# Kernel tuning notes

Hardware: AMD Instinct MI355X
Metric: run time of the kernel (lower is better)

The kernel has to match this reference:

```python
import jax, jax.numpy as jnp
import numpy as np

N_NODES = 20000
N_EDGES = 640000
HIDDEN = 128
NUM_FILTERS = 128
NUM_RBF = 50
NUM_LAYERS = 6
MAX_Z = 100
CUTOFF_UPPER = 5.0
CUTOFF_LOWER = 0.0


def _cosine_cutoff(d):
    # torchmd CosineCutoff with cutoff_lower == 0
    c = 0.5 * (jnp.cos(d * jnp.pi / CUTOFF_UPPER) + 1.0)
    return c * (d < CUTOFF_UPPER).astype(d.dtype)


def setup_inputs() -> dict:
    key = jax.random.key(0)
    ks = jax.random.split(key, 16)
    s = 0.05
    z = jax.random.randint(ks[0], (N_NODES,), 0, MAX_Z)
    pos = jax.random.uniform(ks[1], (N_NODES, 3), dtype=jnp.float32) * 3.0
    src = jax.random.randint(ks[2], (N_EDGES,), 0, N_NODES)
    off = jax.random.randint(ks[3], (N_EDGES,), 1, N_NODES)
    dst = (src + off) % N_NODES  # no self loops -> d > 0 a.s.
    edge_index = jnp.stack([src, dst])
    batch = jnp.zeros((N_NODES,), dtype=jnp.int32)
    # expnorm RBF initial params (ExpNormalSmearing._initial_params)
    start = float(np.exp(-CUTOFF_UPPER + CUTOFF_LOWER))
    rbf_means = jnp.linspace(start, 1.0, NUM_RBF, dtype=jnp.float32)
    rbf_betas = jnp.full((NUM_RBF,), (2.0 / NUM_RBF * (1.0 - start)) ** -2, dtype=jnp.float32)

    def w(k, shape):
        return jax.random.normal(k, shape, dtype=jnp.float32) * s

    L = NUM_LAYERS
    return dict(
        z=z, pos=pos, edge_index=edge_index, batch=batch,
        emb_table=w(ks[4], (MAX_Z, HIDDEN)),
        nbr_emb_table=w(ks[5], (MAX_Z, HIDDEN)),
        nbr_proj_W=w(ks[6], (NUM_RBF, HIDDEN)),
        nbr_proj_b=jnp.zeros((HIDDEN,), jnp.float32),
        combine_W=w(ks[7], (2 * HIDDEN, HIDDEN)),
        combine_b=jnp.zeros((HIDDEN,), jnp.float32),
        rbf_means=rbf_means, rbf_betas=rbf_betas,
        mlp_W1=w(ks[8], (L, NUM_RBF, NUM_FILTERS)),
        mlp_b1=jnp.zeros((L, NUM_FILTERS), jnp.float32),
        mlp_W2=w(ks[9], (L, NUM_FILTERS, NUM_FILTERS)),
        mlp_b2=jnp.zeros((L, NUM_FILTERS), jnp.float32),
        lin1_W=w(ks[10], (L, HIDDEN, NUM_FILTERS)),
        lin2_W=w(ks[11], (L, NUM_FILTERS, HIDDEN)),
        lin2_b=jnp.zeros((L, HIDDEN), jnp.float32),
        lin_W=w(ks[12], (L, HIDDEN, HIDDEN)),
        lin_b=jnp.zeros((L, HIDDEN), jnp.float32),
    )


def reference(z, pos, edge_index, batch, emb_table, nbr_emb_table,
              nbr_proj_W, nbr_proj_b, combine_W, combine_b,
              rbf_means, rbf_betas,
              mlp_W1, mlp_b1, mlp_W2, mlp_b2,
              lin1_W, lin2_W, lin2_b, lin_W, lin_b):
    src, dst = edge_index[0], edge_index[1]
    # Distance (loop=False): edge_vec = pos[src] - pos[dst]
    vec = pos[src] - pos[dst]                      # [E, 3]
    d = jnp.sqrt(jnp.sum(vec * vec, axis=-1))      # [E]
    C = _cosine_cutoff(d)                          # [E]
    alpha = 5.0 / (CUTOFF_UPPER - CUTOFF_LOWER)
    # ExpNormalSmearing: C(d) * exp(-beta * (exp(alpha*(-d+low)) - mu)^2)
    edge_attr = C[:, None] * jnp.exp(
        -rbf_betas * (jnp.exp(alpha * (-d[:, None] + CUTOFF_LOWER)) - rbf_means) ** 2
    )                                              # [E, R]
    x = emb_table[z]                               # [N, H]
    # NeighborEmbedding (self-loop edges masked out, add aggregation)
    nl_mask = (src != dst).astype(x.dtype)
    Wn = (edge_attr @ nbr_proj_W + nbr_proj_b) * (C * nl_mask)[:, None]  # [E, H]
    xn = nbr_emb_table[z]
    agg = jax.ops.segment_sum(xn[src] * Wn, dst, num_segments=N_NODES)
    x = jnp.concatenate([x, agg], axis=1) @ combine_W + combine_b

    def layer(xc, p):
        W1, b1, W2, b2, l1W, l2W, l2b, lW, lb = p
        # CFConv filter: MLP(edge_attr) * cosine_cutoff
        Wf = (jax.nn.silu(edge_attr @ W1 + b1) @ W2 + b2) * C[:, None]   # [E, F]
        h = xc @ l1W                                                      # [N, F]
        ag = jax.ops.segment_sum(h[src] * Wf, dst, num_segments=N_NODES)  # scatter-add
        h = jax.nn.silu(ag @ l2W + l2b)
        h = h @ lW + lb
        return xc + h, None

    x, _ = jax.lax.scan(layer, x, (mlp_W1, mlp_b1, mlp_W2, mlp_b2,
                                   lin1_W, lin2_W, lin2_b, lin_W, lin_b))
    return x
```

## Files before the change

### kernel.cpp

```cpp
#include <hip/hip_runtime.h>
#include <hip/hip_bf16.h>
#include <math.h>

#define NN 20000
#define NE 640000
#define H  128
#define RB 50
#define NL 6
#define TBINS 4096

typedef unsigned short u16;
typedef __attribute__((ext_vector_type(8))) short short8v;
typedef __attribute__((ext_vector_type(4))) float f32x4;

__device__ __forceinline__ u16 f2b(float v) {
  unsigned x = __float_as_uint(v);
  unsigned r = (x + 0x7FFFu + ((x >> 16) & 1u)) >> 16;
  return (u16)r;
}
__device__ __forceinline__ float b2f(u16 u) {
  return __uint_as_float(((unsigned int)u) << 16);
}

__global__ void k_zero_i32(int* __restrict__ p, int n) {
  int i = blockIdx.x * blockDim.x + threadIdx.x;
  if (i < n) p[i] = 0;
}
__global__ void k_hist(const int* __restrict__ ei, int* __restrict__ counts) {
  int e = blockIdx.x * blockDim.x + threadIdx.x;
  if (e < NE) atomicAdd(&counts[ei[NE + e]], 1);
}
__global__ __launch_bounds__(1024) void k_scan(const int* __restrict__ counts,
                                               int* __restrict__ cursor) {
  __shared__ int tsum[1024];
  int tid = threadIdx.x;
  int base = tid * 20;
  int s = 0;
  #pragma unroll
  for (int j = 0; j < 20; ++j) {
    int i = base + j;
    s += (i < NN) ? counts[i] : 0;
  }
  tsum[tid] = s;
  __syncthreads();
  for (int off = 1; off < 1024; off <<= 1) {
    int t = (tid >= off) ? tsum[tid - off] : 0;
    __syncthreads();
    tsum[tid] += t;
    __syncthreads();
  }
  int run = (tid > 0) ? tsum[tid - 1] : 0;
  #pragma unroll
  for (int j = 0; j < 20; ++j) {
    int i = base + j;
    if (i < NN) { cursor[i] = run; run += counts[i]; }
  }
}
__global__ void k_place(const int* __restrict__ ei, int* __restrict__ cursor,
                        int* __restrict__ perm) {
  int e = blockIdx.x * blockDim.x + threadIdx.x;
  if (e < NE) {
    int d = ei[NE + e];
    int p = atomicAdd(&cursor[d], 1);
    perm[p] = e;
  }
}

__global__ void k_edge(const int* __restrict__ ei, const int* __restrict__ perm,
                       const float* __restrict__ pos,
                       int* __restrict__ srcS, int* __restrict__ dstS,
                       float* __restrict__ tvS) {
  int p = blockIdx.x * 256 + threadIdx.x;
  if (p >= NE) return;
  int e = perm[p];
  int s = ei[e], t = ei[NE + e];
  srcS[p] = s; dstS[p] = t;
  float dx = pos[3*s]   - pos[3*t];
  float dy = pos[3*s+1] - pos[3*t+1];
  float dz = pos[3*s+2] - pos[3*t+2];
  float d = sqrtf(dx*dx + dy*dy + dz*dz);
  tvS[p] = expf(-d);
}

__global__ __launch_bounds__(256) void k_tbuild(
    const float* __restrict__ means, const float* __restrict__ betas,
    const float* __restrict__ npW, const float* __restrict__ npb,
    const float* __restrict__ W1, const float* __restrict__ b1,
    const float* __restrict__ W2, const float* __restrict__ b2,
    u16* __restrict__ tb)
{
  int t  = blockIdx.x / (TBINS / 32);
  int j0 = (blockIdx.x % (TBINS / 32)) * 32;
  __shared__ float sAttr[32][52];
  __shared__ float sCut[32];
  __shared__ float sT[32][132];
  int tid = threadIdx.x;
  float tv0 = expf(-5.f);
  float dtv = (1.f - tv0) / (float)(TBINS - 1);
  for (int idx = tid; idx < 32 * RB; idx += 256) {
    int r = idx / RB, k = idx % RB;
    float tv = tv0 + (j0 + r) * dtv;
    float d = -logf(tv);
    float C = 0.5f * (cosf(d * 0.628318530717958647692f) + 1.f);
    if (d >= 5.f) C = 0.f;
    float diff = tv - means[k];
    sAttr[r][k] = C * expf(-betas[k] * diff * diff);
    if (k == 0) sCut[r] = C;
  }
  __syncthreads();
  int g = tid >> 5, c0 = (tid & 31) * 4, eb = g * 4;
  float acc[4][4];
  #pragma unroll
  for (int i = 0; i < 4; ++i)
    for (int j = 0; j < 4; ++j) acc[i][j] = 0.f;
  const float* Wa = (t == 0) ? npW : (W1 + (size_t)(t - 1) * RB * H);
  for (int k = 0; k < RB; ++k) {
    float4 wv = *(const float4*)&Wa[(size_t)k * H + c0];
    #pragma unroll
    for (int i = 0; i < 4; ++i) {
      float a = sAttr[eb + i][k];
      acc[i][0] += a * wv.x; acc[i][1] += a * wv.y;
      acc[i][2] += a * wv.z; acc[i][3] += a * wv.w;
    }
  }
  size_t obase = (size_t)t * TBINS * H;
  int pb = (c0 & 15) * 8 + (c0 >> 4);
  if (t == 0) {
    float4 b4 = *(const float4*)&npb[c0];
    float bvA[4] = {b4.x, b4.y, b4.z, b4.w};
    #pragma unroll
    for (int i = 0; i < 4; ++i) {
      float Cv = sCut[eb + i];
      size_t rb = obase + (size_t)(j0 + eb + i) * H;
      #pragma unroll
      for (int j = 0; j < 4; ++j)
        tb[rb + pb + 8 * j] = f2b((acc[i][j] + bvA[j]) * Cv);
    }
  } else {
    float4 b4 = *(const float4*)&b1[(size_t)(t - 1) * H + c0];
    float bvA[4] = {b4.x, b4.y, b4.z, b4.w};
    #pragma unroll
    for (int i = 0; i < 4; ++i) {
      #pragma unroll
      for (int j = 0; j < 4; ++j) {
        float v = acc[i][j] + bvA[j];
        sT[eb + i][c0 + j] = v / (1.f + __expf(-v));
      }
    }
    __syncthreads();
    #pragma unroll
    for (int i = 0; i < 4; ++i)
      for (int j = 0; j < 4; ++j) acc[i][j] = 0.f;
    const float* Wb = W2 + (size_t)(t - 1) * H * H;
    for (int k = 0; k < H; ++k) {
      float4 wv = *(const float4*)&Wb[(size_t)k * H + c0];
      #pragma unroll
      for (int i = 0; i < 4; ++i) {
        float a = sT[eb + i][k];
        acc[i][0] += a * wv.x; acc[i][1] += a * wv.y;
        acc[i][2] += a * wv.z; acc[i][3] += a * wv.w;
      }
    }
    float4 b24 = *(const float4*)&b2[(size_t)(t - 1) * H + c0];
    float bvB[4] = {b24.x, b24.y, b24.z, b24.w};
    #pragma unroll
    for (int i = 0; i < 4; ++i) {
      float Cv = sCut[eb + i];
      size_t rb = obase + (size_t)(j0 + eb + i) * H;
      #pragma unroll
      for (int j = 0; j < 4; ++j)
        tb[rb + pb + 8 * j] = f2b((acc[i][j] + bvB[j]) * Cv);
    }
  }
}

__global__ void k_prepw2(const float* __restrict__ l2W, const float* __restrict__ lW,
                         const float* __restrict__ l1W, u16* __restrict__ wt) {
  int i = blockIdx.x * 256 + threadIdx.x;
  if (i >= 3 * NL * 128 * 136) return;
  int a = i / (NL * 128 * 136);
  int r = i % (NL * 128 * 136);
  int l = r / (128 * 136);
  int r2 = r % (128 * 136);
  int n = r2 / 136, k = r2 % 136;
  const float* src = (a == 0) ? l2W : (a == 1) ? lW : l1W;
  wt[i] = (k < H) ? f2b(src[(size_t)l * H * H + (size_t)k * H + n]) : (u16)0;
}

__global__ void k_embed(const int* __restrict__ z, const float* __restrict__ emb,
                        const float* __restrict__ nemb,
                        float* __restrict__ x, u16* __restrict__ xnb,
                        float* __restrict__ aggz) {
  int i = blockIdx.x * blockDim.x + threadIdx.x;
  if (i >= NN * H) return;
  int n = i >> 7, c = i & (H - 1);
  long o = (long)z[n] * H + c;
  x[i] = emb[o];
  xnb[(size_t)n * H + ((c & 15) * 8 + (c >> 4))] = f2b(nemb[o]);
  aggz[i] = 0.f;
}

__global__ __launch_bounds__(256) void k_es(
    const int* __restrict__ srcS, const int* __restrict__ dstS,
    const float* __restrict__ tvS, const u16* __restrict__ tb,
    const u16* __restrict__ hsrc, float* __restrict__ agg, int maskSelf)
{
  int tid = threadIdx.x;
  int lane = tid & 63, wv = tid >> 6;
  int r16 = lane & 15, g4 = lane >> 4;
  int g16 = g4 * 16;
  long ebase = (long)blockIdx.x * 512 + wv * 128 + g4 * 32;
  int srcR_A = srcS[ebase + r16];
  int dstR_A = dstS[ebase + r16];
  float tvR_A = tvS[ebase + r16];
  int srcR_B = srcS[ebase + 16 + r16];
  int dstR_B = dstS[ebase + 16 + r16];
  float tvR_B = tvS[ebase + 16 + r16];
  float tv0 = expf(-5.f);
  float inv = (float)(TBINS - 1) / (1.f - tv0);
  float vsumA[8], vsumB[8];
  #pragma unroll
  for (int ct = 0; ct < 8; ++ct) { vsumA[ct] = 0.f; vsumB[ct] = 0.f; }
  int pdstA = -1, pdstB = -1;
#define DECLS(P) int P##_s, P##_d; float P##_w; short8v P##_hv, P##_lo, P##_hi;
  DECLS(A0) DECLS(A1) DECLS(A2) DECLS(B0) DECLS(B1) DECLS(B2)
#define ISSUE(P, R, ii) { \
    P##_s = __shfl(srcR_##R, g16 + (ii), 64); \
    P##_d = __shfl(dstR_##R, g16 + (ii), 64); \
    float tvv = __shfl(tvR_##R, g16 + (ii), 64); \
    P##_hv = *(const short8v*)&hsrc[(size_t)P##_s * H + r16 * 8]; \
    float u = fminf(fmaxf((tvv - tv0) * inv, 0.f), (float)(TBINS - 1) - 1e-3f); \
    int jj = (int)u; P##_w = u - (float)jj; \
    P##_lo = *(const short8v*)&tb[(size_t)jj * H + r16 * 8]; \
    P##_hi = *(const short8v*)&tb[(size_t)(jj + 1) * H + r16 * 8]; }
#define CONSUME(P, R) { \
    float m = (maskSelf && P##_s == P##_d) ? 0.f : 1.f; \
    if (P##_d != pdst##R) { \
      if (pdst##R >= 0) { \
        float* ap = agg + (size_t)pdst##R * H + r16; \
        _Pragma("unroll") \
        for (int ct = 0; ct < 8; ++ct) atomicAdd(ap + ct * 16, vsum##R[ct]); \
      } \
      _Pragma("unroll") \
      for (int ct = 0; ct < 8; ++ct) vsum##R[ct] = 0.f; \
      pdst##R = P##_d; \
    } \
    _Pragma("unroll") \
    for (int ct = 0; ct < 8; ++ct) { \
      float lo = b2f((u16)P##_lo[ct]); \
      float hi = b2f((u16)P##_hi[ct]); \
      vsum##R[ct] += (lo + P##_w * (hi - lo)) * m * b2f((u16)P##_hv[ct]); \
    } }
  ISSUE(A0, A, 0); ISSUE(B0, B, 0);
  ISSUE(A1, A, 1); ISSUE(B1, B, 1);
  ISSUE(A2, A, 2); ISSUE(B2, B, 2);
  #pragma unroll
  for (int i = 0; i < 16; ++i) {
    int ph = i % 3;
    if (ph == 0) {
      CONSUME(A0, A); if (i + 3 < 16) ISSUE(A0, A, i + 3);
      CONSUME(B0, B); if (i + 3 < 16) ISSUE(B0, B, i + 3);
    } else if (ph == 1) {
      CONSUME(A1, A); if (i + 3 < 16) ISSUE(A1, A, i + 3);
      CONSUME(B1, B); if (i + 3 < 16) ISSUE(B1, B, i + 3);
    } else {
      CONSUME(A2, A); if (i + 3 < 16) ISSUE(A2, A, i + 3);
      CONSUME(B2, B); if (i + 3 < 16) ISSUE(B2, B, i + 3);
    }
  }
#undef ISSUE
#undef CONSUME
#undef DECLS
  if (pdstA >= 0) {
    float* ap = agg + (size_t)pdstA * H + r16;
    #pragma unroll
    for (int ct = 0; ct < 8; ++ct) atomicAdd(ap + ct * 16, vsumA[ct]);
  }
  if (pdstB >= 0) {
    float* ap = agg + (size_t)pdstB * H + r16;
    #pragma unroll
    for (int ct = 0; ct < 8; ++ct) atomicAdd(ap + ct * 16, vsumB[ct]);
  }
}

__global__ __launch_bounds__(256) void k_combine(
    const float* __restrict__ xb, float* __restrict__ ag,
    const float* __restrict__ cW, const float* __restrict__ cb,
    const float* __restrict__ l1W0, float* __restrict__ xout,
    u16* __restrict__ hb)
{
  __shared__ float sX[32][132];
  __shared__ float sG[32][132];
  int tid = threadIdx.x;
  int n0 = blockIdx.x * 32;
  #pragma unroll
  for (int j = 0; j < 4; ++j) {
    int f4 = tid + j * 256;
    int r = f4 >> 5, c4 = f4 & 31;
    *(float4*)&sX[r][c4 * 4] = *(const float4*)&xb[(size_t)(n0 + r) * H + c4 * 4];
    *(float4*)&sG[r][c4 * 4] = *(const float4*)&ag[(size_t)(n0 + r) * H + c4 * 4];
    *(float4*)&ag[(size_t)(n0 + r) * H + c4 * 4] = make_float4(0.f, 0.f, 0.f, 0.f);
  }
  __syncthreads();
  int g = tid >> 5;
  int c0 = (tid & 31) * 4;
  int eb = g * 4;
  float acc[4][4];
  #pragma unroll
  for (int i = 0; i < 4; ++i)
    for (int j = 0; j < 4; ++j) acc[i][j] = 0.f;
  for (int k = 0; k < H; ++k) {
    float4 wv = *(const float4*)&cW[(size_t)k * H + c0];
    #pragma unroll
    for (int i = 0; i < 4; ++i) {
      float a = sX[eb + i][k];
      acc[i][0] += a * wv.x; acc[i][1] += a * wv.y;
      acc[i][2] += a * wv.z; acc[i][3] += a * wv.w;
    }
  }
  for (int k = 0; k < H; ++k) {
    float4 wv = *(const float4*)&cW[(size_t)(H + k) * H + c0];
    #pragma unroll
    for (int i = 0; i < 4; ++i) {
      float a = sG[eb + i][k];
      acc[i][0] += a * wv.x; acc[i][1] += a * wv.y;
      acc[i][2] += a * wv.z; acc[i][3] += a * wv.w;
    }
  }
  float4 bv = *(const float4*)&cb[c0];
  __syncthreads();
  #pragma unroll
  for (int i = 0; i < 4; ++i) {
    int n = n0 + eb + i;
    float o0 = acc[i][0] + bv.x, o1 = acc[i][1] + bv.y;
    float o2 = acc[i][2] + bv.z, o3 = acc[i][3] + bv.w;
    *(float4*)&xout[(size_t)n * H + c0] = make_float4(o0, o1, o2, o3);
    sX[eb + i][c0] = o0; sX[eb + i][c0+1] = o1;
    sX[eb + i][c0+2] = o2; sX[eb + i][c0+3] = o3;
  }
  __syncthreads();
  #pragma unroll
  for (int i = 0; i < 4; ++i)
    for (int j = 0; j < 4; ++j) acc[i][j] = 0.f;
  for (int k = 0; k < H; ++k) {
    float4 wv = *(const float4*)&l1W0[(size_t)k * H + c0];
    #pragma unroll
    for (int i = 0; i < 4; ++i) {
      float a = sX[eb + i][k];
      acc[i][0] += a * wv.x; acc[i][1] += a * wv.y;
      acc[i][2] += a * wv.z; acc[i][3] += a * wv.w;
    }
  }
  int pbase = (c0 & 15) * 8 + (c0 >> 4);
  #pragma unroll
  for (int i = 0; i < 4; ++i) {
    int n = n0 + eb + i;
    #pragma unroll
    for (int j = 0; j < 4; ++j)
      hb[(size_t)n * H + pbase + 8 * j] = f2b(acc[i][j]);
  }
}

__global__ __launch_bounds__(256) void k_gemmM(
    float* __restrict__ A, const u16* __restrict__ W2t, const float* __restrict__ b2,
    const u16* __restrict__ W3t, const float* __restrict__ b3,
    const float* __restrict__ xin, float* __restrict__ xout,
    const u16* __restrict__ l1Wnt, u16* __restrict__ hb)
{
  __shared__ __align__(16) u16 sA[64 * 136];
  __shared__ __align__(16) u16 sT[64 * 136];
  int tid = threadIdx.x;
  int lane = tid & 63, wv = tid >> 6;
  int r16 = lane & 15, g4 = lane >> 4;
  int n0 = blockIdx.x * 64;
  #pragma unroll
  for (int j = 0; j < 8; ++j) {
    int f4 = tid + j * 256;
    int r = f4 >> 5, c4 = f4 & 31;
    int n = n0 + r;
    float4 v = make_float4(0.f, 0.f, 0.f, 0.f);
    if (n < NN) {
      v = *(const float4*)&A[(size_t)n * H + c4 * 4];
      *(float4*)&A[(size_t)n * H + c4 * 4] = make_float4(0.f, 0.f, 0.f, 0.f);
    }
    unsigned lo = (unsigned)f2b(v.x) | ((unsigned)f2b(v.y) << 16);
    unsigned hi = (unsigned)f2b(v.z) | ((unsigned)f2b(v.w) << 16);
    *(unsigned*)&sA[r * 136 + c4 * 4]     = lo;
    *(unsigned*)&sA[r * 136 + c4 * 4 + 2] = hi;
  }
  __syncthreads();
  int wrow = wv * 16;
  f32x4 acc[8];
  #pragma unroll
  for (int ct = 0; ct < 8; ++ct) acc[ct] = (f32x4){0.f, 0.f, 0.f, 0.f};
  #pragma unroll
  for (int kt = 0; kt < 4; ++kt) {
    short8v aF = *(const short8v*)&sA[(wrow + r16) * 136 + kt * 32 + g4 * 8];
    #pragma unroll
    for (int ct = 0; ct < 8; ++ct) {
      short8v bF = *(const short8v*)&W2t[(ct * 16 + r16) * 136 + kt * 32 + g4 * 8];
      acc[ct] = __builtin_amdgcn_mfma_f32_16x16x32_bf16(aF, bF, acc[ct], 0, 0, 0);
    }
  }
  #pragma unroll
  for (int ct = 0; ct < 8; ++ct) {
    float bb = b2[ct * 16 + r16];
    #pragma unroll
    for (int r = 0; r < 4; ++r) {
      float v = acc[ct][r] + bb;
      v = v / (1.f + __expf(-v));
      sT[(wrow + g4 * 4 + r) * 136 + ct * 16 + r16] = f2b(v);
    }
  }
  #pragma unroll
  for (int ct = 0; ct < 8; ++ct) acc[ct] = (f32x4){0.f, 0.f, 0.f, 0.f};
  #pragma unroll
  for (int kt = 0; kt < 4; ++kt) {
    short8v aF = *(const short8v*)&sT[(wrow + r16) * 136 + kt * 32 + g4 * 8];
    #pragma unroll
    for (int ct = 0; ct < 8; ++ct) {
      short8v bF = *(const short8v*)&W3t[(ct * 16 + r16) * 136 + kt * 32 + g4 * 8];
      acc[ct] = __builtin_amdgcn_mfma_f32_16x16x32_bf16(aF, bF, acc[ct], 0, 0, 0);
    }
  }
  #pragma unroll
  for (int ct = 0; ct < 8; ++ct) {
    float bb = b3[ct * 16 + r16];
    #pragma unroll
    for (int r = 0; r < 4; ++r) {
      int n = n0 + wrow + g4 * 4 + r;
      if (n < NN) {
        float o = acc[ct][r] + bb + xin[(size_t)n * H + ct * 16 + r16];
        xout[(size_t)n * H + ct * 16 + r16] = o;
        sA[(wrow + g4 * 4 + r) * 136 + ct * 16 + r16] = f2b(o);
      }
    }
  }
  if (!l1Wnt) return;
  #pragma unroll
  for (int ct = 0; ct < 8; ++ct) acc[ct] = (f32x4){0.f, 0.f, 0.f, 0.f};
  #pragma unroll
  for (int kt = 0; kt < 4; ++kt) {
    short8v aF = *(const short8v*)&sA[(wrow + r16) * 136 + kt * 32 + g4 * 8];
    #pragma unroll
    for (int ct = 0; ct < 8; ++ct) {
      short8v bF = *(const short8v*)&l1Wnt[(ct * 16 + r16) * 136 + kt * 32 + g4 * 8];
      acc[ct] = __builtin_amdgcn_mfma_f32_16x16x32_bf16(aF, bF, acc[ct], 0, 0, 0);
    }
  }
  #pragma unroll
  for (int r = 0; r < 4; ++r) {
    int n = n0 + wrow + g4 * 4 + r;
    if (n < NN) {
      short8v hv;
      #pragma unroll
      for (int ct = 0; ct < 8; ++ct) hv[ct] = (short)f2b(acc[ct][r]);
      *(short8v*)&hb[(size_t)n * H + r16 * 8] = hv;
    }
  }
}

extern "C" void kernel_launch(void* const* d_in, const int* in_sizes, int n_in,
                              void* d_out, int out_size, void* d_ws, size_t ws_size,
                              hipStream_t stream) {
  int bo = (n_in >= 4 && in_sizes[3] == NN) ? 0 : -1;
  const int*   z     = (const int*)d_in[0];
  const float* pos   = (const float*)d_in[1];
  const int*   ei    = (const int*)d_in[2];
  const float* emb   = (const float*)d_in[4 + bo];
  const float* nemb  = (const float*)d_in[5 + bo];
  const float* npW   = (const float*)d_in[6 + bo];
  const float* npb   = (const float*)d_in[7 + bo];
  const float* cW    = (const float*)d_in[8 + bo];
  const float* cb    = (const float*)d_in[9 + bo];
  const float* means = (const float*)d_in[10 + bo];
  const float* betas = (const float*)d_in[11 + bo];
  const float* W1    = (const float*)d_in[12 + bo];
  const float* b1    = (const float*)d_in[13 + bo];
  const float* W2    = (const float*)d_in[14 + bo];
  const float* b2    = (const float*)d_in[15 + bo];
  const float* l1W   = (const float*)d_in[16 + bo];
  const float* l2W   = (const float*)d_in[17 + bo];
  const float* l2b   = (const float*)d_in[18 + bo];
  const float* lW    = (const float*)d_in[19 + bo];
  const float* lb    = (const float*)d_in[20 + bo];

  char* w = (char*)d_ws;
  auto alloc = [&](size_t bytes) { char* p = w; w += (bytes + 255) & ~(size_t)255; return p; };
  int*   counts = (int*)  alloc((size_t)NN * 4);
  int*   cursor = (int*)  alloc((size_t)NN * 4);
  int*   perm   = (int*)  alloc((size_t)NE * 4);
  int*   srcS   = (int*)  alloc((size_t)NE * 4);
  int*   dstS   = (int*)  alloc((size_t)NE * 4);
  float* tvS    = (float*)alloc((size_t)NE * 4);
  u16*   tb     = (u16*)  alloc((size_t)7 * TBINS * H * 2);
  u16*   wt     = (u16*)  alloc((size_t)3 * NL * 128 * 136 * 2);
  float* xbuf   = (float*)alloc((size_t)NN * H * 4);
  float* agg    = (float*)alloc((size_t)NN * H * 4);
  u16*   xnb    = (u16*)  alloc((size_t)NN * H * 2);
  u16*   hbuf   = (u16*)  alloc((size_t)NN * H * 2);

  u16* l2Wt = wt;
  u16* lWt  = wt + (size_t)NL * 128 * 136;
  u16* l1Wt = wt + (size_t)2 * NL * 128 * 136;

  dim3 b256(256);
  int gE256 = (NE + 255) / 256;
  int gNH   = (NN * H + 255) / 256;
  int gES   = NE / 512;
  int gG    = NN / 32;
  int gM    = (NN + 63) / 64;
  int gTB   = 7 * (TBINS / 32);
  int gPW   = (3 * NL * 128 * 136 + 255) / 256;

  k_zero_i32<<<(NN + 255) / 256, b256, 0, stream>>>(counts, NN);
  k_hist<<<gE256, b256, 0, stream>>>(ei, counts);
  k_scan<<<1, 1024, 0, stream>>>(counts, cursor);
  k_place<<<gE256, b256, 0, stream>>>(ei, cursor, perm);
  k_edge<<<gE256, b256, 0, stream>>>(ei, perm, pos, srcS, dstS, tvS);
  k_tbuild<<<gTB, b256, 0, stream>>>(means, betas, npW, npb, W1, b1, W2, b2, tb);
  k_prepw2<<<gPW, b256, 0, stream>>>(l2W, lW, l1W, wt);
  k_embed<<<gNH, b256, 0, stream>>>(z, emb, nemb, xbuf, xnb, agg);

  k_es<<<gES, b256, 0, stream>>>(srcS, dstS, tvS, tb, xnb, agg, 1);
  k_combine<<<gG, b256, 0, stream>>>(xbuf, agg, cW, cb, l1W, xbuf, hbuf);

  for (int l = 0; l < NL; ++l) {
    k_es<<<gES, b256, 0, stream>>>(srcS, dstS, tvS,
                                   tb + (size_t)(1 + l) * TBINS * H,
                                   hbuf, agg, 0);
    const u16* l1Wnt = (l + 1 < NL) ? (l1Wt + (size_t)(l + 1) * 128 * 136) : nullptr;
    float* xo = (l == NL - 1) ? (float*)d_out : xbuf;
    k_gemmM<<<gM, b256, 0, stream>>>(agg, l2Wt + (size_t)l * 128 * 136, l2b + (size_t)l * H,
                                     lWt + (size_t)l * 128 * 136, lb + (size_t)l * H,
                                     xbuf, xo, l1Wnt, hbuf);
  }
}
```

Baseline: 683.2 us.

## Replace atomic edge scatter with per-node CSR gather and MFMA combine

The edge aggregation kernel now assigns 16 threads per destination node and walks that node's CSR edge range from counts/cursor. It writes the sum directly, so the float atomics, the dstS array and the zeroing of agg in the embed and GEMM kernels are no longer needed. The combine step is rewritten as a bf16 MFMA kernel using pre-transposed weights produced in prep. The risk is load imbalance across nodes with varying degree, plus bf16 rounding in the combine GEMM, which was fp32 before.

```diff
diff --git a/kernel.cpp b/kernel.cpp
--- a/kernel.cpp
+++ b/kernel.cpp
@@ -68,13 +68,12 @@
 
 __global__ void k_edge(const int* __restrict__ ei, const int* __restrict__ perm,
                        const float* __restrict__ pos,
-                       int* __restrict__ srcS, int* __restrict__ dstS,
-                       float* __restrict__ tvS) {
+                       int* __restrict__ srcS, float* __restrict__ tvS) {
   int p = blockIdx.x * 256 + threadIdx.x;
   if (p >= NE) return;
   int e = perm[p];
   int s = ei[e], t = ei[NE + e];
-  srcS[p] = s; dstS[p] = t;
+  srcS[p] = s;
   float dx = pos[3*s]   - pos[3*t];
   float dy = pos[3*s+1] - pos[3*t+1];
   float dz = pos[3*s+2] - pos[3*t+2];
@@ -174,195 +173,177 @@
   }
 }
 
+#define WBLK (128 * 136)
 __global__ void k_prepw2(const float* __restrict__ l2W, const float* __restrict__ lW,
-                         const float* __restrict__ l1W, u16* __restrict__ wt) {
+                         const float* __restrict__ l1W, const float* __restrict__ cW,
+                         u16* __restrict__ wt) {
   int i = blockIdx.x * 256 + threadIdx.x;
-  if (i >= 3 * NL * 128 * 136) return;
-  int a = i / (NL * 128 * 136);
-  int r = i % (NL * 128 * 136);
-  int l = r / (128 * 136);
-  int r2 = r % (128 * 136);
-  int n = r2 / 136, k = r2 % 136;
-  const float* src = (a == 0) ? l2W : (a == 1) ? lW : l1W;
-  wt[i] = (k < H) ? f2b(src[(size_t)l * H * H + (size_t)k * H + n]) : (u16)0;
+  if (i >= (3 * NL + 2) * WBLK) return;
+  if (i < 3 * NL * WBLK) {
+    int a = i / (NL * WBLK);
+    int r = i % (NL * WBLK);
+    int l = r / WBLK;
+    int r2 = r % WBLK;
+    int n = r2 / 136, k = r2 % 136;
+    const float* src = (a == 0) ? l2W : (a == 1) ? lW : l1W;
+    wt[i] = (k < H) ? f2b(src[(size_t)l * H * H + (size_t)k * H + n]) : (u16)0;
+  } else {
+    int j = i - 3 * NL * WBLK;
+    int which = j / WBLK;
+    int r2 = j % WBLK;
+    int n = r2 / 136, k = r2 % 136;
+    wt[i] = (k < H) ? f2b(cW[(size_t)(which * 128 + k) * H + n]) : (u16)0;
+  }
 }
 
 __global__ void k_embed(const int* __restrict__ z, const float* __restrict__ emb,
                         const float* __restrict__ nemb,
-                        float* __restrict__ x, u16* __restrict__ xnb,
-                        float* __restrict__ aggz) {
+                        float* __restrict__ x, u16* __restrict__ xnb) {
   int i = blockIdx.x * blockDim.x + threadIdx.x;
   if (i >= NN * H) return;
   int n = i >> 7, c = i & (H - 1);
   long o = (long)z[n] * H + c;
   x[i] = emb[o];
   xnb[(size_t)n * H + ((c & 15) * 8 + (c >> 4))] = f2b(nemb[o]);
-  aggz[i] = 0.f;
-}
-
-__global__ __launch_bounds__(256) void k_es(
-    const int* __restrict__ srcS, const int* __restrict__ dstS,
-    const float* __restrict__ tvS, const u16* __restrict__ tb,
-    const u16* __restrict__ hsrc, float* __restrict__ agg, int maskSelf)
+}
+
+__global__ __launch_bounds__(256) void k_eso(
+    const int* __restrict__ counts, const int* __restrict__ cursor,
+    const int* __restrict__ srcS, const float* __restrict__ tvS,
+    const u16* __restrict__ tb, const u16* __restrict__ hsrc,
+    float* __restrict__ agg, int maskSelf)
 {
   int tid = threadIdx.x;
-  int lane = tid & 63, wv = tid >> 6;
-  int r16 = lane & 15, g4 = lane >> 4;
-  int g16 = g4 * 16;
-  long ebase = (long)blockIdx.x * 512 + wv * 128 + g4 * 32;
-  int srcR_A = srcS[ebase + r16];
-  int dstR_A = dstS[ebase + r16];
-  float tvR_A = tvS[ebase + r16];
-  int srcR_B = srcS[ebase + 16 + r16];
-  int dstR_B = dstS[ebase + 16 + r16];
-  float tvR_B = tvS[ebase + 16 + r16];
+  int n = blockIdx.x * 16 + (tid >> 4);
+  int r16 = tid & 15;
+  int cnt = counts[n];
+  long e0 = (long)cursor[n] - cnt;
   float tv0 = expf(-5.f);
   float inv = (float)(TBINS - 1) / (1.f - tv0);
-  float vsumA[8], vsumB[8];
-  #pragma unroll
-  for (int ct = 0; ct < 8; ++ct) { vsumA[ct] = 0.f; vsumB[ct] = 0.f; }
-  int pdstA = -1, pdstB = -1;
-#define DECLS(P) int P##_s, P##_d; float P##_w; short8v P##_hv, P##_lo, P##_hi;
-  DECLS(A0) DECLS(A1) DECLS(A2) DECLS(B0) DECLS(B1) DECLS(B2)
-#define ISSUE(P, R, ii) { \
-    P##_s = __shfl(srcR_##R, g16 + (ii), 64); \
-    P##_d = __shfl(dstR_##R, g16 + (ii), 64); \
-    float tvv = __shfl(tvR_##R, g16 + (ii), 64); \
+  float vsum[8];
+  #pragma unroll
+  for (int ct = 0; ct < 8; ++ct) vsum[ct] = 0.f;
+  int P0_s = 0, P1_s = 0, P2_s = 0;
+  float P0_w = 0.f, P1_w = 0.f, P2_w = 0.f;
+  short8v P0_hv, P0_lo, P0_hi, P1_hv, P1_lo, P1_hi, P2_hv, P2_lo, P2_hi;
+#define ISSUE(P, ii) { int _i = (ii); if (_i < cnt) { \
+    long e = e0 + _i; \
+    P##_s = srcS[e]; float tvv = tvS[e]; \
     P##_hv = *(const short8v*)&hsrc[(size_t)P##_s * H + r16 * 8]; \
     float u = fminf(fmaxf((tvv - tv0) * inv, 0.f), (float)(TBINS - 1) - 1e-3f); \
     int jj = (int)u; P##_w = u - (float)jj; \
     P##_lo = *(const short8v*)&tb[(size_t)jj * H + r16 * 8]; \
-    P##_hi = *(const short8v*)&tb[(size_t)(jj + 1) * H + r16 * 8]; }
-#define CONSUME(P, R) { \
-    float m = (maskSelf && P##_s == P##_d) ? 0.f : 1.f; \
-    if (P##_d != pdst##R) { \
-      if (pdst##R >= 0) { \
-        float* ap = agg + (size_t)pdst##R * H + r16; \
-        _Pragma("unroll") \
-        for (int ct = 0; ct < 8; ++ct) atomicAdd(ap + ct * 16, vsum##R[ct]); \
-      } \
-      _Pragma("unroll") \
-      for (int ct = 0; ct < 8; ++ct) vsum##R[ct] = 0.f; \
-      pdst##R = P##_d; \
-    } \
+    P##_hi = *(const short8v*)&tb[(size_t)(jj + 1) * H + r16 * 8]; } }
+#define CONSUME(P) { \
+    float m = (maskSelf && P##_s == n) ? 0.f : 1.f; \
     _Pragma("unroll") \
     for (int ct = 0; ct < 8; ++ct) { \
       float lo = b2f((u16)P##_lo[ct]); \
       float hi = b2f((u16)P##_hi[ct]); \
-      vsum##R[ct] += (lo + P##_w * (hi - lo)) * m * b2f((u16)P##_hv[ct]); \
+      vsum[ct] += (lo + P##_w * (hi - lo)) * m * b2f((u16)P##_hv[ct]); \
     } }
-  ISSUE(A0, A, 0); ISSUE(B0, B, 0);
-  ISSUE(A1, A, 1); ISSUE(B1, B, 1);
-  ISSUE(A2, A, 2); ISSUE(B2, B, 2);
-  #pragma unroll
-  for (int i = 0; i < 16; ++i) {
-    int ph = i % 3;
-    if (ph == 0) {
-      CONSUME(A0, A); if (i + 3 < 16) ISSUE(A0, A, i + 3);
-      CONSUME(B0, B); if (i + 3 < 16) ISSUE(B0, B, i + 3);
-    } else if (ph == 1) {
-      CONSUME(A1, A); if (i + 3 < 16) ISSUE(A1, A, i + 3);
-      CONSUME(B1, B); if (i + 3 < 16) ISSUE(B1, B, i + 3);
-    } else {
-      CONSUME(A2, A); if (i + 3 < 16) ISSUE(A2, A, i + 3);
-      CONSUME(B2, B); if (i + 3 < 16) ISSUE(B2, B, i + 3);
-    }
+  ISSUE(P0, 0); ISSUE(P1, 1); ISSUE(P2, 2);
+  for (int i = 0; i < cnt; i += 3) {
+    CONSUME(P0); ISSUE(P0, i + 3);
+    if (i + 1 < cnt) { CONSUME(P1); ISSUE(P1, i + 4); }
+    if (i + 2 < cnt) { CONSUME(P2); ISSUE(P2, i + 5); }
   }
 #undef ISSUE
 #undef CONSUME
-#undef DECLS
-  if (pdstA >= 0) {
-    float* ap = agg + (size_t)pdstA * H + r16;
-    #pragma unroll
-    for (int ct = 0; ct < 8; ++ct) atomicAdd(ap + ct * 16, vsumA[ct]);
-  }
-  if (pdstB >= 0) {
-    float* ap = agg + (size_t)pdstB * H + r16;
-    #pragma unroll
-    for (int ct = 0; ct < 8; ++ct) atomicAdd(ap + ct * 16, vsumB[ct]);
-  }
-}
-
-__global__ __launch_bounds__(256) void k_combine(
-    const float* __restrict__ xb, float* __restrict__ ag,
-    const float* __restrict__ cW, const float* __restrict__ cb,
-    const float* __restrict__ l1W0, float* __restrict__ xout,
-    u16* __restrict__ hb)
+  float* ap = agg + (size_t)n * H + r16;
+  #pragma unroll
+  for (int ct = 0; ct < 8; ++ct) ap[ct * 16] = vsum[ct];
+}
+
+__global__ __launch_bounds__(256) void k_combineM(
+    const float* __restrict__ xb, const float* __restrict__ ag,
+    const u16* __restrict__ cWt0, const u16* __restrict__ cWt1,
+    const float* __restrict__ cb, const u16* __restrict__ l1W0t,
+    float* __restrict__ xout, u16* __restrict__ hb)
 {
-  __shared__ float sX[32][132];
-  __shared__ float sG[32][132];
+  __shared__ __align__(16) u16 sX[64 * 136];
+  __shared__ __align__(16) u16 sG[64 * 136];
   int tid = threadIdx.x;
-  int n0 = blockIdx.x * 32;
-  #pragma unroll
-  for (int j = 0; j < 4; ++j) {
+  int lane = tid & 63, wv = tid >> 6;
+  int r16 = lane & 15, g4 = lane >> 4;
+  int n0 = blockIdx.x * 64;
+  #pragma unroll
+  for (int j = 0; j < 8; ++j) {
     int f4 = tid + j * 256;
     int r = f4 >> 5, c4 = f4 & 31;
-    *(float4*)&sX[r][c4 * 4] = *(const float4*)&xb[(size_t)(n0 + r) * H + c4 * 4];
-    *(float4*)&sG[r][c4 * 4] = *(const float4*)&ag[(size_t)(n0 + r) * H + c4 * 4];
-    *(float4*)&ag[(size_t)(n0 + r) * H + c4 * 4] = make_float4(0.f, 0.f, 0.f, 0.f);
+    int n = n0 + r;
+    float4 vx = make_float4(0.f, 0.f, 0.f, 0.f);
+    float4 vg = make_float4(0.f, 0.f, 0.f, 0.f);
+    if (n < NN) {
+      vx = *(const float4*)&xb[(size_t)n * H + c4 * 4];
+      vg = *(const float4*)&ag[(size_t)n * H + c4 * 4];
+    }
+    *(unsigned*)&sX[r * 136 + c4 * 4]     = (unsigned)f2b(vx.x) | ((unsigned)f2b(vx.y) << 16);
+    *(unsigned*)&sX[r * 136 + c4 * 4 + 2] = (unsigned)f2b(vx.z) | ((unsigned)f2b(vx.w) << 16);
+    *(unsigned*)&sG[r * 136 + c4 * 4]     = (unsigned)f2b(vg.x) | ((unsigned)f2b(vg.y) << 16);
+    *(unsigned*)&sG[r * 136 + c4 * 4 + 2] = (unsigned)f2b(vg.z) | ((unsigned)f2b(vg.w) << 16);
   }
   __syncthreads();
-  int g = tid >> 5;
-  int c0 = (tid & 31) * 4;
-  int eb = g * 4;
-  float acc[4][4];
-  #pragma unroll
-  for (int i = 0; i < 4; ++i)
-    for (int j = 0; j < 4; ++j) acc[i][j] = 0.f;
-  for (int k = 0; k < H; ++k) {
-    float4 wv = *(const float4*)&cW[(size_t)k * H + c0];
-    #pragma unroll
-    for (int i = 0; i < 4; ++i) {
-      float a = sX[eb + i][k];
-      acc[i][0] += a * wv.x; acc[i][1] += a * wv.y;
-      acc[i][2] += a * wv.z; acc[i][3] += a * wv.w;
-    }
-  }
-  for (int k = 0; k < H; ++k) {
-    float4 wv = *(const float4*)&cW[(size_t)(H + k) * H + c0];
-    #pragma unroll
-    for (int i = 0; i < 4; ++i) {
-      float a = sG[eb + i][k];
-      acc[i][0] += a * wv.x; acc[i][1] += a * wv.y;
-      acc[i][2] += a * wv.z; acc[i][3] += a * wv.w;
-    }
-  }
-  float4 bv = *(const float4*)&cb[c0];
-  __syncthreads();
-  #pragma unroll
-  for (int i = 0; i < 4; ++i) {
-    int n = n0 + eb + i;
-    float o0 = acc[i][0] + bv.x, o1 = acc[i][1] + bv.y;
-    float o2 = acc[i][2] + bv.z, o3 = acc[i][3] + bv.w;
-    *(float4*)&xout[(size_t)n * H + c0] = make_float4(o0, o1, o2, o3);
-    sX[eb + i][c0] = o0; sX[eb + i][c0+1] = o1;
-    sX[eb + i][c0+2] = o2; sX[eb + i][c0+3] = o3;
-  }
-  __syncthreads();
-  #pragma unroll
-  for (int i = 0; i < 4; ++i)
-    for (int j = 0; j < 4; ++j) acc[i][j] = 0.f;
-  for (int k = 0; k < H; ++k) {
-    float4 wv = *(const float4*)&l1W0[(size_t)k * H + c0];
-    #pragma unroll
-    for (int i = 0; i < 4; ++i) {
-      float a = sX[eb + i][k];
-      acc[i][0] += a * wv.x; acc[i][1] += a * wv.y;
-      acc[i][2] += a * wv.z; acc[i][3] += a * wv.w;
-    }
-  }
-  int pbase = (c0 & 15) * 8 + (c0 >> 4);
-  #pragma unroll
-  for (int i = 0; i < 4; ++i) {
-    int n = n0 + eb + i;
-    #pragma unroll
-    for (int j = 0; j < 4; ++j)
-      hb[(size_t)n * H + pbase + 8 * j] = f2b(acc[i][j]);
+  int wrow = wv * 16;
+  f32x4 acc[8];
+  #pragma unroll
+  for (int ct = 0; ct < 8; ++ct) acc[ct] = (f32x4){0.f, 0.f, 0.f, 0.f};
+  #pragma unroll
+  for (int kt = 0; kt < 4; ++kt) {
+    short8v aF = *(const short8v*)&sX[(wrow + r16) * 136 + kt * 32 + g4 * 8];
+    #pragma unroll
+    for (int ct = 0; ct < 8; ++ct) {
+      short8v bF = *(const short8v*)&cWt0[(ct * 16 + r16) * 136 + kt * 32 + g4 * 8];
+      acc[ct] = __builtin_amdgcn_mfma_f32_16x16x32_bf16(aF, bF, acc[ct], 0, 0, 0);
+    }
+  }
+  #pragma unroll
+  for (int kt = 0; kt < 4; ++kt) {
+    short8v aF = *(const short8v*)&sG[(wrow + r16) * 136 + kt * 32 + g4 * 8];
+    #pragma unroll
+    for (int ct = 0; ct < 8; ++ct) {
+      short8v bF = *(const short8v*)&cWt1[(ct * 16 + r16) * 136 + kt * 32 + g4 * 8];
+      acc[ct] = __builtin_amdgcn_mfma_f32_16x16x32_bf16(aF, bF, acc[ct], 0, 0, 0);
+    }
+  }
+  #pragma unroll
+  for (int ct = 0; ct < 8; ++ct) {
+    float bb = cb[ct * 16 + r16];
+    #pragma unroll
+    for (int r = 0; r < 4; ++r) {
+      int n = n0 + wrow + g4 * 4 + r;
+      if (n < NN) {
+        float o = acc[ct][r] + bb;
+        xout[(size_t)n * H + ct * 16 + r16] = o;
+        sX[(wrow + g4 * 4 + r) * 136 + ct * 16 + r16] = f2b(o);
+      }
+    }
+  }
+  #pragma unroll
+  for (int ct = 0; ct < 8; ++ct) acc[ct] = (f32x4){0.f, 0.f, 0.f, 0.f};
+  #pragma unroll
+  for (int kt = 0; kt < 4; ++kt) {
+    short8v aF = *(const short8v*)&sX[(wrow + r16) * 136 + kt * 32 + g4 * 8];
+    #pragma unroll
+    for (int ct = 0; ct < 8; ++ct) {
+      short8v bF = *(const short8v*)&l1W0t[(ct * 16 + r16) * 136 + kt * 32 + g4 * 8];
+      acc[ct] = __builtin_amdgcn_mfma_f32_16x16x32_bf16(aF, bF, acc[ct], 0, 0, 0);
+    }
+  }
+  #pragma unroll
+  for (int r = 0; r < 4; ++r) {
+    int n = n0 + wrow + g4 * 4 + r;
+    if (n < NN) {
+      short8v hv;
+      #pragma unroll
+      for (int ct = 0; ct < 8; ++ct) hv[ct] = (short)f2b(acc[ct][r]);
+      *(short8v*)&hb[(size_t)n * H + r16 * 8] = hv;
+    }
   }
 }
 
 __global__ __launch_bounds__(256) void k_gemmM(
-    float* __restrict__ A, const u16* __restrict__ W2t, const float* __restrict__ b2,
+    const float* __restrict__ A, const u16* __restrict__ W2t, const float* __restrict__ b2,
     const u16* __restrict__ W3t, const float* __restrict__ b3,
     const float* __restrict__ xin, float* __restrict__ xout,
     const u16* __restrict__ l1Wnt, u16* __restrict__ hb)
@@ -379,14 +360,9 @@
     int r = f4 >> 5, c4 = f4 & 31;
     int n = n0 + r;
     float4 v = make_float4(0.f, 0.f, 0.f, 0.f);
-    if (n < NN) {
-      v = *(const float4*)&A[(size_t)n * H + c4 * 4];
-      *(float4*)&A[(size_t)n * H + c4 * 4] = make_float4(0.f, 0.f, 0.f, 0.f);
-    }
-    unsigned lo = (unsigned)f2b(v.x) | ((unsigned)f2b(v.y) << 16);
-    unsigned hi = (unsigned)f2b(v.z) | ((unsigned)f2b(v.w) << 16);
-    *(unsigned*)&sA[r * 136 + c4 * 4]     = lo;
-    *(unsigned*)&sA[r * 136 + c4 * 4 + 2] = hi;
+    if (n < NN) v = *(const float4*)&A[(size_t)n * H + c4 * 4];
+    *(unsigned*)&sA[r * 136 + c4 * 4]     = (unsigned)f2b(v.x) | ((unsigned)f2b(v.y) << 16);
+    *(unsigned*)&sA[r * 136 + c4 * 4 + 2] = (unsigned)f2b(v.z) | ((unsigned)f2b(v.w) << 16);
   }
   __syncthreads();
   int wrow = wv * 16;
@@ -491,48 +467,48 @@
   int*   cursor = (int*)  alloc((size_t)NN * 4);
   int*   perm   = (int*)  alloc((size_t)NE * 4);
   int*   srcS   = (int*)  alloc((size_t)NE * 4);
-  int*   dstS   = (int*)  alloc((size_t)NE * 4);
   float* tvS    = (float*)alloc((size_t)NE * 4);
   u16*   tb     = (u16*)  alloc((size_t)7 * TBINS * H * 2);
-  u16*   wt     = (u16*)  alloc((size_t)3 * NL * 128 * 136 * 2);
+  u16*   wt     = (u16*)  alloc((size_t)(3 * NL + 2) * WBLK * 2);
   float* xbuf   = (float*)alloc((size_t)NN * H * 4);
   float* agg    = (float*)alloc((size_t)NN * H * 4);
   u16*   xnb    = (u16*)  alloc((size_t)NN * H * 2);
   u16*   hbuf   = (u16*)  alloc((size_t)NN * H * 2);
 
   u16* l2Wt = wt;
-  u16* lWt  = wt + (size_t)NL * 128 * 136;
-  u16* l1Wt = wt + (size_t)2 * NL * 128 * 136;
+  u16* lWt  = wt + (size_t)NL * WBLK;
+  u16* l1Wt = wt + (size_t)2 * NL * WBLK;
+  u16* cWt0 = wt + (size_t)3 * NL * WBLK;
+  u16* cWt1 = cWt0 + WBLK;
 
   dim3 b256(256);
   int gE256 = (NE + 255) / 256;
   int gNH   = (NN * H + 255) / 256;
-  int gES   = NE / 512;
-  int gG    = NN / 32;
+  int gESO  = NN / 16;
   int gM    = (NN + 63) / 64;
   int gTB   = 7 * (TBINS / 32);
-  int gPW   = (3 * NL * 128 * 136 + 255) / 256;
+  int gPW   = ((3 * NL + 2) * WBLK + 255) / 256;
 
   k_zero_i32<<<(NN + 255) / 256, b256, 0, stream>>>(counts, NN);
   k_hist<<<gE256, b256, 0, stream>>>(ei, counts);
   k_scan<<<1, 1024, 0, stream>>>(counts, cursor);
   k_place<<<gE256, b256, 0, stream>>>(ei, cursor, perm);
-  k_edge<<<gE256, b256, 0, stream>>>(ei, perm, pos, srcS, dstS, tvS);
+  k_edge<<<gE256, b256, 0, stream>>>(ei, perm, pos, srcS, tvS);
   k_tbuild<<<gTB, b256, 0, stream>>>(means, betas, npW, npb, W1, b1, W2, b2, tb);
-  k_prepw2<<<gPW, b256, 0, stream>>>(l2W, lW, l1W, wt);
-  k_embed<<<gNH, b256, 0, stream>>>(z, emb, nemb, xbuf, xnb, agg);
-
-  k_es<<<gES, b256, 0, stream>>>(srcS, dstS, tvS, tb, xnb, agg, 1);
-  k_combine<<<gG, b256, 0, stream>>>(xbuf, agg, cW, cb, l1W, xbuf, hbuf);
+  k_prepw2<<<gPW, b256, 0, stream>>>(l2W, lW, l1W, cW, wt);
+  k_embed<<<gNH, b256, 0, stream>>>(z, emb, nemb, xbuf, xnb);
+
+  k_eso<<<gESO, b256, 0, stream>>>(counts, cursor, srcS, tvS, tb, xnb, agg, 1);
+  k_combineM<<<gM, b256, 0, stream>>>(xbuf, agg, cWt0, cWt1, cb, l1Wt, xbuf, hbuf);
 
   for (int l = 0; l < NL; ++l) {
-    k_es<<<gES, b256, 0, stream>>>(srcS, dstS, tvS,
-                                   tb + (size_t)(1 + l) * TBINS * H,
-                                   hbuf, agg, 0);
-    const u16* l1Wnt = (l + 1 < NL) ? (l1Wt + (size_t)(l + 1) * 128 * 136) : nullptr;
+    k_eso<<<gESO, b256, 0, stream>>>(counts, cursor, srcS, tvS,
+                                     tb + (size_t)(1 + l) * TBINS * H,
+                                     hbuf, agg, 0);
+    const u16* l1Wnt = (l + 1 < NL) ? (l1Wt + (size_t)(l + 1) * WBLK) : nullptr;
     float* xo = (l == NL - 1) ? (float*)d_out : xbuf;
-    k_gemmM<<<gM, b256, 0, stream>>>(agg, l2Wt + (size_t)l * 128 * 136, l2b + (size_t)l * H,
-                                     lWt + (size_t)l * 128 * 136, lb + (size_t)l * H,
+    k_gemmM<<<gM, b256, 0, stream>>>(agg, l2Wt + (size_t)l * WBLK, l2b + (size_t)l * H,
+                                     lWt + (size_t)l * WBLK, lb + (size_t)l * H,
                                      xbuf, xo, l1Wnt, hbuf);
   }
 }
```

Measured after the change: 674.9 us. About the same (-1.2%).
